# Kernel optimization log

Measured on AMD Instinct MI355X. Metric: run time of the kernel, lower is better.

The kernel has to match this reference:

```python
import jax, jax.numpy as jnp
import numpy as np

EPS = 1e-05


def setup_inputs() -> dict:
    key = jax.random.key(0)
    B, T, C = 8, 8192, 512
    x = jax.random.normal(key, (B, T, C), dtype=jnp.float32)
    # Learned per-channel scale; module initializes it to ones.
    weight = jnp.ones((C,), dtype=jnp.float32)
    return {"x": x, "weight": weight}


def reference(x, weight):
    """Cumulative (running) group norm over the frame axis.

    x: [B, T, C]; stats are accumulated over channels AND all frames <= t.
    """
    input_dtype = x.dtype
    xc = x.astype(jnp.float32)
    B, T, C = xc.shape

    # Per-frame channel sum, then cumulative sum over time -> [B, T, 1]
    cum_sum = jnp.cumsum(jnp.sum(xc, axis=-1, keepdims=True), axis=1)
    # Element count up to frame t: (t+1) * C (mask is all-ones here)
    cum_count = (jnp.arange(1, T + 1, dtype=jnp.float32) * C).reshape(1, T, 1)
    cum_count = jnp.maximum(cum_count, 1.0)

    cum_mean = cum_sum / cum_count  # [B, T, 1]

    # Squared deviation from the *running* mean, summed over channels, cumsum over time.
    sq_diff = jnp.square(xc - cum_mean)  # [B, T, C]
    cum_var = jnp.cumsum(jnp.sum(sq_diff, axis=-1, keepdims=True), axis=1) / cum_count

    normalized = (xc - cum_mean) * jax.lax.rsqrt(cum_var + EPS)
    out = normalized * weight.astype(jnp.float32)  # broadcast over [B, T, C]
    return out.astype(input_dtype)
```

## Files before the change

kernel.cpp:

```cpp
#include <hip/hip_runtime.h>

#define EPS 1e-5f

typedef float nfloat4 __attribute__((ext_vector_type(4)));


__global__ __launch_bounds__(256) void frame_stats_kernel(
    const float* __restrict__ x, float* __restrict__ s_arr,
    float* __restrict__ q_arr) {
  const int wave = threadIdx.x >> 6;
  const int lane = threadIdx.x & 63;
  const int frame = blockIdx.x * 4 + wave;
  const nfloat4* xb = (const nfloat4*)(x + (size_t)frame * 512);
  nfloat4 a = xb[lane];
  nfloat4 b = xb[64 + lane];
  float s = a.x + a.y + a.z + a.w + b.x + b.y + b.z + b.w;
  float q = a.x * a.x + a.y * a.y + a.z * a.z + a.w * a.w +
            b.x * b.x + b.y * b.y + b.z * b.z + b.w * b.w;
#pragma unroll
  for (int off = 32; off >= 1; off >>= 1) {
    s += __shfl_down(s, off);
    q += __shfl_down(q, off);
  }
  if (lane == 0) {
    s_arr[frame] = s;
    q_arr[frame] = q;
  }
}

__global__ __launch_bounds__(1024) void scan_apply_kernel(
    const float* __restrict__ x, const float* __restrict__ w,
    const float* __restrict__ s_arr, const float* __restrict__ q_arr,
    float* __restrict__ out) {
  const int T = 8192;
  const int tid = threadIdx.x;
  const int lane = tid & 63;
  const int wid = tid >> 6;
  const int b = blockIdx.x >> 6;
  const int slice = blockIdx.x & 63;

  __shared__ float lds_s[16];
  __shared__ float lds_v[16];
  __shared__ float lds_m[128];
  __shared__ float lds_i[128];

  const nfloat4* s4p = (const nfloat4*)(s_arr + (size_t)b * T);
  const nfloat4* q4p = (const nfloat4*)(q_arr + (size_t)b * T);

  nfloat4 sa = s4p[2 * tid];
  nfloat4 sb = s4p[2 * tid + 1];
  nfloat4 qa = q4p[2 * tid];
  nfloat4 qb = q4p[2 * tid + 1];

  float p0 = sa.x;
  float p1 = p0 + sa.y;
  float p2 = p1 + sa.z;
  float p3 = p2 + sa.w;
  float p4 = p3 + sb.x;
  float p5 = p4 + sb.y;
  float p6 = p5 + sb.z;
  float p7 = p6 + sb.w;
  float tot = p7, incl = tot;
#pragma unroll
  for (int off = 1; off < 64; off <<= 1) {
    float n = __shfl_up(incl, off);
    if (lane >= off) incl += n;
  }
  if (lane == 63) lds_s[wid] = incl;
  __syncthreads();
  float waveExcl = 0.f;
#pragma unroll
  for (int wv = 0; wv < 16; ++wv)
    if (wv < wid) waveExcl += lds_s[wv];
  float base = waveExcl + incl - tot;

  const int t0 = tid << 3;
  float c0 = (float)(t0 + 1) * 512.f;
  float c1 = (float)(t0 + 2) * 512.f;
  float c2 = (float)(t0 + 3) * 512.f;
  float c3 = (float)(t0 + 4) * 512.f;
  float c4 = (float)(t0 + 5) * 512.f;
  float c5 = (float)(t0 + 6) * 512.f;
  float c6 = (float)(t0 + 7) * 512.f;
  float c7 = (float)(t0 + 8) * 512.f;
  float m0 = (base + p0) / c0;
  float m1 = (base + p1) / c1;
  float m2 = (base + p2) / c2;
  float m3 = (base + p3) / c3;
  float m4 = (base + p4) / c4;
  float m5 = (base + p5) / c5;
  float m6 = (base + p6) / c6;
  float m7 = (base + p7) / c7;

  float v0 = qa.x - 2.f * m0 * sa.x + 512.f * m0 * m0;
  float v1 = qa.y - 2.f * m1 * sa.y + 512.f * m1 * m1;
  float v2 = qa.z - 2.f * m2 * sa.z + 512.f * m2 * m2;
  float v3 = qa.w - 2.f * m3 * sa.w + 512.f * m3 * m3;
  float v4 = qb.x - 2.f * m4 * sb.x + 512.f * m4 * m4;
  float v5 = qb.y - 2.f * m5 * sb.y + 512.f * m5 * m5;
  float v6 = qb.z - 2.f * m6 * sb.z + 512.f * m6 * m6;
  float v7 = qb.w - 2.f * m7 * sb.w + 512.f * m7 * m7;

  float r0 = v0;
  float r1 = r0 + v1;
  float r2 = r1 + v2;
  float r3 = r2 + v3;
  float r4 = r3 + v4;
  float r5 = r4 + v5;
  float r6 = r5 + v6;
  float r7 = r6 + v7;
  float totv = r7, inclv = totv;
#pragma unroll
  for (int off = 1; off < 64; off <<= 1) {
    float n = __shfl_up(inclv, off);
    if (lane >= off) inclv += n;
  }
  if (lane == 63) lds_v[wid] = inclv;
  __syncthreads();
  float waveExclV = 0.f;
#pragma unroll
  for (int wv = 0; wv < 16; ++wv)
    if (wv < wid) waveExclV += lds_v[wv];
  float baseV = waveExclV + inclv - totv;

  const int sliceFirstThread = slice << 4;
  if ((tid >> 4) == slice) {
    const int k = (tid - sliceFirstThread) << 3;
    lds_m[k + 0] = m0;
    lds_m[k + 1] = m1;
    lds_m[k + 2] = m2;
    lds_m[k + 3] = m3;
    lds_m[k + 4] = m4;
    lds_m[k + 5] = m5;
    lds_m[k + 6] = m6;
    lds_m[k + 7] = m7;
    lds_i[k + 0] = rsqrtf((baseV + r0) / c0 + EPS);
    lds_i[k + 1] = rsqrtf((baseV + r1) / c1 + EPS);
    lds_i[k + 2] = rsqrtf((baseV + r2) / c2 + EPS);
    lds_i[k + 3] = rsqrtf((baseV + r3) / c3 + EPS);
    lds_i[k + 4] = rsqrtf((baseV + r4) / c4 + EPS);
    lds_i[k + 5] = rsqrtf((baseV + r5) / c5 + EPS);
    lds_i[k + 6] = rsqrtf((baseV + r6) / c6 + EPS);
    lds_i[k + 7] = rsqrtf((baseV + r7) / c7 + EPS);
  }
  __syncthreads();

  const size_t base4 = ((size_t)b * 8192 + (size_t)slice * 128) * 128;
  const nfloat4 wv4 = ((const nfloat4*)w)[tid & 127];
  const nfloat4* x4 = (const nfloat4*)x;
  nfloat4* out4 = (nfloat4*)out;
#pragma unroll 4
  for (int k = 0; k < 16; ++k) {
    const size_t idx = base4 + (size_t)(k << 10) + tid;
    const int frame_local = (int)((idx >> 7) & 127) ;
    nfloat4 xv = x4[idx];
    const float m = lds_m[(k << 3) + (tid >> 7)];
    const float iv = lds_i[(k << 3) + (tid >> 7)];
    (void)frame_local;
    nfloat4 o;
    o.x = (xv.x - m) * iv * wv4.x;
    o.y = (xv.y - m) * iv * wv4.y;
    o.z = (xv.z - m) * iv * wv4.z;
    o.w = (xv.w - m) * iv * wv4.w;
    __builtin_nontemporal_store(o, out4 + idx);
  }
}

extern "C" void kernel_launch(void* const* d_in, const int* in_sizes, int n_in,
                              void* d_out, int out_size, void* d_ws,
                              size_t ws_size, hipStream_t stream) {
  const float* x = (const float*)d_in[0];
  const float* w = (const float*)d_in[1];
  float* out = (float*)d_out;
  const int BT = 65536;

  float* s_arr = (float*)d_ws;
  float* q_arr = s_arr + BT;

  frame_stats_kernel<<<BT / 4, 256, 0, stream>>>(x, s_arr, q_arr);
  scan_apply_kernel<<<512, 1024, 0, stream>>>(x, w, s_arr, q_arr, out);
}
```

Measured before the change: 248.0 us.

## Split scan into per-row scan kernel and separate apply kernel

Before, each of 512 blocks redundantly recomputed the full per-row two-level scan over 8192 frames just to obtain stats for its own 128-frame slice. Now one small kernel per batch row computes the running mean and inverse std and writes them to workspace, and a lightweight 256-thread apply kernel with 2048 blocks normalizes 32 frames per block. This removes 64x redundant scan work, at the cost of an extra launch and a serialized 8-block scan stage that uses little of the GPU.

```diff
diff --git a/kernel.cpp b/kernel.cpp
--- a/kernel.cpp
+++ b/kernel.cpp
@@ -28,21 +28,17 @@
   }
 }
 
-__global__ __launch_bounds__(1024) void scan_apply_kernel(
-    const float* __restrict__ x, const float* __restrict__ w,
+__global__ __launch_bounds__(1024) void row_scan_kernel(
     const float* __restrict__ s_arr, const float* __restrict__ q_arr,
-    float* __restrict__ out) {
+    float* __restrict__ mean_arr, float* __restrict__ inv_arr) {
   const int T = 8192;
   const int tid = threadIdx.x;
   const int lane = tid & 63;
   const int wid = tid >> 6;
-  const int b = blockIdx.x >> 6;
-  const int slice = blockIdx.x & 63;
+  const int b = blockIdx.x;
 
   __shared__ float lds_s[16];
   __shared__ float lds_v[16];
-  __shared__ float lds_m[128];
-  __shared__ float lds_i[128];
 
   const nfloat4* s4p = (const nfloat4*)(s_arr + (size_t)b * T);
   const nfloat4* q4p = (const nfloat4*)(q_arr + (size_t)b * T);
@@ -123,40 +119,51 @@
     if (wv < wid) waveExclV += lds_v[wv];
   float baseV = waveExclV + inclv - totv;
 
-  const int sliceFirstThread = slice << 4;
-  if ((tid >> 4) == slice) {
-    const int k = (tid - sliceFirstThread) << 3;
-    lds_m[k + 0] = m0;
-    lds_m[k + 1] = m1;
-    lds_m[k + 2] = m2;
-    lds_m[k + 3] = m3;
-    lds_m[k + 4] = m4;
-    lds_m[k + 5] = m5;
-    lds_m[k + 6] = m6;
-    lds_m[k + 7] = m7;
-    lds_i[k + 0] = rsqrtf((baseV + r0) / c0 + EPS);
-    lds_i[k + 1] = rsqrtf((baseV + r1) / c1 + EPS);
-    lds_i[k + 2] = rsqrtf((baseV + r2) / c2 + EPS);
-    lds_i[k + 3] = rsqrtf((baseV + r3) / c3 + EPS);
-    lds_i[k + 4] = rsqrtf((baseV + r4) / c4 + EPS);
-    lds_i[k + 5] = rsqrtf((baseV + r5) / c5 + EPS);
-    lds_i[k + 6] = rsqrtf((baseV + r6) / c6 + EPS);
-    lds_i[k + 7] = rsqrtf((baseV + r7) / c7 + EPS);
+  nfloat4 mlo, mhi, ilo, ihi;
+  mlo.x = m0; mlo.y = m1; mlo.z = m2; mlo.w = m3;
+  mhi.x = m4; mhi.y = m5; mhi.z = m6; mhi.w = m7;
+  ilo.x = rsqrtf((baseV + r0) / c0 + EPS);
+  ilo.y = rsqrtf((baseV + r1) / c1 + EPS);
+  ilo.z = rsqrtf((baseV + r2) / c2 + EPS);
+  ilo.w = rsqrtf((baseV + r3) / c3 + EPS);
+  ihi.x = rsqrtf((baseV + r4) / c4 + EPS);
+  ihi.y = rsqrtf((baseV + r5) / c5 + EPS);
+  ihi.z = rsqrtf((baseV + r6) / c6 + EPS);
+  ihi.w = rsqrtf((baseV + r7) / c7 + EPS);
+
+  nfloat4* mrow = (nfloat4*)(mean_arr + (size_t)b * T);
+  nfloat4* irow = (nfloat4*)(inv_arr + (size_t)b * T);
+  mrow[2 * tid] = mlo;
+  mrow[2 * tid + 1] = mhi;
+  irow[2 * tid] = ilo;
+  irow[2 * tid + 1] = ihi;
+}
+
+__global__ __launch_bounds__(256) void apply_kernel(
+    const float* __restrict__ x, const float* __restrict__ w,
+    const float* __restrict__ mean_arr, const float* __restrict__ inv_arr,
+    float* __restrict__ out) {
+  const int tid = threadIdx.x;
+  __shared__ float lds_m[32];
+  __shared__ float lds_i[32];
+  const int f0 = blockIdx.x << 5;
+  if (tid < 32) {
+    lds_m[tid] = mean_arr[f0 + tid];
+    lds_i[tid] = inv_arr[f0 + tid];
   }
   __syncthreads();
 
-  const size_t base4 = ((size_t)b * 8192 + (size_t)slice * 128) * 128;
   const nfloat4 wv4 = ((const nfloat4*)w)[tid & 127];
+  const size_t base4 = (size_t)f0 << 7;
   const nfloat4* x4 = (const nfloat4*)x;
   nfloat4* out4 = (nfloat4*)out;
 #pragma unroll 4
   for (int k = 0; k < 16; ++k) {
-    const size_t idx = base4 + (size_t)(k << 10) + tid;
-    const int frame_local = (int)((idx >> 7) & 127) ;
+    const size_t idx = base4 + (size_t)(k << 8) + (size_t)tid;
+    const int fl = (k << 1) + (tid >> 7);
     nfloat4 xv = x4[idx];
-    const float m = lds_m[(k << 3) + (tid >> 7)];
-    const float iv = lds_i[(k << 3) + (tid >> 7)];
-    (void)frame_local;
+    const float m = lds_m[fl];
+    const float iv = lds_i[fl];
     nfloat4 o;
     o.x = (xv.x - m) * iv * wv4.x;
     o.y = (xv.y - m) * iv * wv4.y;
@@ -176,7 +183,10 @@
 
   float* s_arr = (float*)d_ws;
   float* q_arr = s_arr + BT;
+  float* mean_arr = q_arr + BT;
+  float* inv_arr = mean_arr + BT;
 
   frame_stats_kernel<<<BT / 4, 256, 0, stream>>>(x, s_arr, q_arr);
-  scan_apply_kernel<<<512, 1024, 0, stream>>>(x, w, s_arr, q_arr, out);
+  row_scan_kernel<<<8, 1024, 0, stream>>>(s_arr, q_arr, mean_arr, inv_arr);
+  apply_kernel<<<BT / 32, 256, 0, stream>>>(x, w, mean_arr, inv_arr, out);
 }
```

Result: no change. 249.4 us (+0.6%).
